# Optimization experiments

Measured on AMD Instinct MI355X. Metric: run time of the kernel, lower is better.

## Reference

```python
import jax, jax.numpy as jnp
import numpy as np
from jax import lax

H_ENC = 64
H_DEC = 128
PRED_STEPS = 30


def _run_lstm_last(x, Wih, Whh, bih, bhh):
    """Batched LSTM (batch_first), returns last hidden state. x: [N, T, I] -> [N, H]."""
    N = x.shape[0]
    H = Whh.shape[1]
    xg = jnp.einsum('nti,gi->ntg', x, Wih) + bih  # [N, T, 4H], input projection hoisted

    def step(carry, g_t):
        h, c = carry
        gates = g_t + h @ Whh.T + bhh
        i, f, g, o = jnp.split(gates, 4, axis=-1)  # torch gate order i,f,g,o
        c = jax.nn.sigmoid(f) * c + jax.nn.sigmoid(i) * jnp.tanh(g)
        h = jax.nn.sigmoid(o) * jnp.tanh(c)
        return (h, c), None

    z = jnp.zeros((N, H), x.dtype)
    (h, _), _ = lax.scan(step, (z, z), jnp.swapaxes(xg, 0, 1))
    return h


def setup_inputs() -> dict:
    key = jax.random.key(0)
    ks = jax.random.split(key, 20)
    B, T, NMAX = 2048, 50, 16
    s = 0.1
    inp = {
        'train_agent': jax.random.normal(ks[0], (B, T, 2), jnp.float32),
        'neighbour': jax.random.normal(ks[1], (B, NMAX, T, 2), jnp.float32),
        'neighbour_counts': jax.random.randint(ks[2], (B,), 0, NMAX + 1),
        # agent encoder LSTM(2 -> 64)
        'Wih_a': jax.random.normal(ks[3], (4 * H_ENC, 2), jnp.float32) * s,
        'Whh_a': jax.random.normal(ks[4], (4 * H_ENC, H_ENC), jnp.float32) * s,
        'bih_a': jax.random.normal(ks[5], (4 * H_ENC,), jnp.float32) * s,
        'bhh_a': jax.random.normal(ks[6], (4 * H_ENC,), jnp.float32) * s,
        # neighbour encoder LSTM(2 -> 64)
        'Wih_n': jax.random.normal(ks[7], (4 * H_ENC, 2), jnp.float32) * s,
        'Whh_n': jax.random.normal(ks[8], (4 * H_ENC, H_ENC), jnp.float32) * s,
        'bih_n': jax.random.normal(ks[9], (4 * H_ENC,), jnp.float32) * s,
        'bhh_n': jax.random.normal(ks[10], (4 * H_ENC,), jnp.float32) * s,
        # decoder LSTMCell(128 -> 128)
        'Wih_d': jax.random.normal(ks[11], (4 * H_DEC, H_DEC), jnp.float32) * s,
        'Whh_d': jax.random.normal(ks[12], (4 * H_DEC, H_DEC), jnp.float32) * s,
        'bih_d': jax.random.normal(ks[13], (4 * H_DEC,), jnp.float32) * s,
        'bhh_d': jax.random.normal(ks[14], (4 * H_DEC,), jnp.float32) * s,
        # embedding_pos Linear(128 -> 2)
        'Wpos': jax.random.normal(ks[15], (2, H_DEC), jnp.float32) * s,
        'bpos': jax.random.normal(ks[16], (2,), jnp.float32) * s,
    }
    return inp


def reference(train_agent, neighbour, neighbour_counts,
              Wih_a, Whh_a, bih_a, bhh_a,
              Wih_n, Whh_n, bih_n, bhh_n,
              Wih_d, Whh_d, bih_d, bhh_d,
              Wpos, bpos):
    B, NMAX, T, _ = neighbour.shape

    # agent encoder: last hidden state  [B, 64]
    agent_emb = _run_lstm_last(train_agent, Wih_a, Whh_a, bih_a, bhh_a)

    # neighbour encoder over all padded neighbour sequences  [B*NMAX, 64]
    n_enc = _run_lstm_last(neighbour.reshape(B * NMAX, T, 2),
                           Wih_n, Whh_n, bih_n, bhh_n).reshape(B, NMAX, H_ENC)
    valid = jnp.arange(NMAX)[None, :] < neighbour_counts[:, None]  # [B, NMAX]
    neg_inf = jnp.asarray(-jnp.inf, n_enc.dtype)
    n_max = jnp.max(jnp.where(valid[:, :, None], n_enc, neg_inf), axis=1)  # [B, 64]
    neigh_emb = jnp.where((neighbour_counts > 0)[:, None], n_max,
                          jnp.zeros((), n_enc.dtype))

    # decoder: LSTMCell fed its own hidden state as input, 30 steps
    h0 = jnp.concatenate([agent_emb, neigh_emb], axis=1)  # [B, 128]
    c0 = jnp.zeros_like(h0)

    def dec_step(carry, _):
        h, c = carry
        gates = h @ Wih_d.T + bih_d + h @ Whh_d.T + bhh_d  # input == hidden == h
        i, f, g, o = jnp.split(gates, 4, axis=-1)
        c_new = jax.nn.sigmoid(f) * c + jax.nn.sigmoid(i) * jnp.tanh(g)
        h_new = jax.nn.sigmoid(o) * jnp.tanh(c_new)
        pred = h_new @ Wpos.T + bpos  # [B, 2]
        return (h_new, c_new), pred

    _, preds = lax.scan(dec_step, (h0, c0), None, length=PRED_STEPS)  # [30, B, 2]
    return jnp.swapaxes(preds, 0, 1)  # [B, 30, 2]
```

## Files before the change

kernel.cpp:

```cpp
#include <hip/hip_runtime.h>
#include <stdint.h>


#define T_SEQ 50
#define PRED_STEPS 30
#define NMAX 16

typedef float v2f __attribute__((ext_vector_type(2)));
typedef float v4f __attribute__((ext_vector_type(4)));
typedef short v8s __attribute__((ext_vector_type(8)));

#define L2E 1.44269504f
#define L2E2 2.88539008f

static constexpr size_t OFF_AEMB  = 0;
static constexpr size_t OFF_NENC  = 131072;
static constexpr size_t OFF_IDX   = 2228224;
static constexpr size_t OFF_PACKA = 2490368;
static constexpr size_t OFF_PACKN = 2498560;
static constexpr size_t OFF_WDP   = 2506752;
static constexpr size_t OFF_WDB   = 2539520;

__device__ __forceinline__ float frcp(float x) { return __builtin_amdgcn_rcpf(x); }
#if __has_builtin(__builtin_amdgcn_exp2f)
__device__ __forceinline__ float fexp2(float x) { return __builtin_amdgcn_exp2f(x); }
#else
__device__ __forceinline__ float fexp2(float x) { return exp2f(x); }
#endif
__device__ __forceinline__ unsigned bf16rne(float f) {
  unsigned u = __float_as_uint(f);
  u += 0x7fff + ((u >> 16) & 1);
  return u >> 16;
}
__device__ __forceinline__ v4f mfma16(v8s a, v8s b, v4f c) {
  return __builtin_amdgcn_mfma_f32_16x16x32_bf16(a, b, c, 0, 0, 0);
}

__device__ __forceinline__ float cell_update(float iv, float fv, float gv,
                                             float ov, float& cref) {
  float ef = fexp2(-fv);
  float ei = fexp2(-iv);
  float eg = fexp2(-gv);
  float t1 = (1.f + ei) * (1.f + eg);
  float rD = frcp((1.f + ef) * t1);
  float sf = t1 * rD;
  float u  = (1.f - eg) * ((1.f + ef) * rD);
  float cn = fmaf(sf, cref, u);
  cref = cn;
  float eo = fexp2(-ov);
  float ec = fexp2(fminf(-L2E2 * cn, 60.f));
  return (1.f - ec) * frcp((1.f + eo) * (1.f + ec));
}

__device__ __forceinline__ uint4 pack8(const float* __restrict__ p, float gs) {
  float4 w0 = *(const float4*)p;
  float4 w1 = *(const float4*)(p + 4);
  uint4 o;
  o.x = bf16rne(w0.x * gs) | (bf16rne(w0.y * gs) << 16);
  o.y = bf16rne(w0.z * gs) | (bf16rne(w0.w * gs) << 16);
  o.z = bf16rne(w1.x * gs) | (bf16rne(w1.y * gs) << 16);
  o.w = bf16rne(w1.z * gs) | (bf16rne(w1.w * gs) << 16);
  return o;
}
__device__ __forceinline__ uint4 pack8sum(const float* __restrict__ pa,
                                          const float* __restrict__ pb, float gs) {
  float4 a0 = *(const float4*)pa, a1 = *(const float4*)(pa + 4);
  float4 b0 = *(const float4*)pb, b1 = *(const float4*)(pb + 4);
  uint4 o;
  o.x = bf16rne((a0.x + b0.x) * gs) | (bf16rne((a0.y + b0.y) * gs) << 16);
  o.y = bf16rne((a0.z + b0.z) * gs) | (bf16rne((a0.w + b0.w) * gs) << 16);
  o.z = bf16rne((a1.x + b1.x) * gs) | (bf16rne((a1.y + b1.y) * gs) << 16);
  o.w = bf16rne((a1.z + b1.z) * gs) | (bf16rne((a1.w + b1.w) * gs) << 16);
  return o;
}

__global__ void prep_kernel(const float* __restrict__ Whh_a, const float* __restrict__ Whh_n,
                            const float* __restrict__ Wih_d, const float* __restrict__ Whh_d,
                            const float* __restrict__ bih_d, const float* __restrict__ bhh_d,
                            uint4* __restrict__ packA, uint4* __restrict__ packN,
                            uint4* __restrict__ packD, float* __restrict__ bd,
                            int* __restrict__ idxb) {
  const int b = blockIdx.x;
  {
    const int gi = b * 256 + threadIdx.x;
    for (int i = gi; i < 32768; i += 12288) idxb[i] = -1;
    if (gi == 0) idxb[32768] = 0;
  }
  if (b < 16) {
    const int which = b >> 3;
    const float* Whh = which ? Whh_n : Whh_a;
    uint4* dst = which ? packN : packA;
    const int idx = (b & 7) * 256 + threadIdx.x;
    const int lane = idx & 63, c = idx >> 6;
    const int kh = c & 1, g = (c >> 1) & 3, w = c >> 3;
    const float gs = (g == 2) ? L2E2 : L2E;
    const int row = g * 64 + 16 * w + (lane & 15);
    const int kb = kh * 32 + (lane >> 4) * 8;
    dst[c * 64 + lane] = pack8(Whh + row * 64 + kb, gs);
  } else {
    const int idx = (b - 16) * 256 + threadIdx.x;
    const int lane = idx & 63, c = idx >> 6;
    const int kh = c & 3, i = (c >> 2) & 1, wv = c >> 3;
    const int g = wv & 3, q = wv >> 2;
    const float gs = (g == 2) ? L2E2 : L2E;
    const int ju = q * 32 + i * 16 + (lane & 15);
    const int row = g * 128 + ju;
    const int kb = kh * 32 + (lane >> 4) * 8;
    packD[c * 64 + lane] = pack8sum(Wih_d + row * 128 + kb, Whh_d + row * 128 + kb, gs);
    if (b < 18) {
      int iB = (b - 16) * 256 + threadIdx.x;
      float s = ((iB >> 7) == 2) ? L2E2 : L2E;
      bd[iB] = (bih_d[iB] + bhh_d[iB]) * s;
    }
  }
}

__global__ void compact_kernel(const int* __restrict__ cnts, int* __restrict__ idxb) {
  const int b = blockIdx.x * 256 + threadIdx.x;
  if (b >= 2048) return;
  int cnt = cnts[b];
  cnt = cnt < 0 ? 0 : (cnt > NMAX ? NMAX : cnt);
  if (cnt == 0) return;
  int pos = atomicAdd(idxb + 32768, cnt);
  for (int j = 0; j < cnt; ++j) idxb[pos + j] = b * NMAX + j;
}

__global__ __launch_bounds__(256, 4) void enc_mfma_kernel(
    const float* __restrict__ xA, const float* __restrict__ xN,
    const v8s* __restrict__ packA, const v8s* __restrict__ packN,
    const float* __restrict__ Wih_a, const float* __restrict__ bih_a, const float* __restrict__ bhh_a,
    const float* __restrict__ Wih_n, const float* __restrict__ bih_n, const float* __restrict__ bhh_n,
    const int* __restrict__ idxb,
    float* __restrict__ outA, float* __restrict__ outN) {
  __shared__ unsigned short hph[2304];
  __shared__ float xst[1600];
  __shared__ int sidx[16];
  const int tid = threadIdx.x, lane = tid & 63, wv = tid >> 6;
  const int nb = blockIdx.x;
  const bool isA = nb >= 2048;
  const int s0 = (isA ? nb - 2048 : nb) * 16;

  if (!isA && s0 >= idxb[32768]) return;

  const float* xsrc = isA ? xA : xN;
  const v8s* pk = isA ? packA : packN;
  const float* Wih = isA ? Wih_a : Wih_n;
  const float* bih = isA ? bih_a : bih_n;
  const float* bhh = isA ? bhh_a : bhh_n;
  float* outp = isA ? outA : outN;

  v8s B[4][2];
#pragma unroll
  for (int g = 0; g < 4; ++g)
#pragma unroll
    for (int kh = 0; kh < 2; ++kh)
      B[g][kh] = pk[(wv * 8 + g * 2 + kh) * 64 + lane];

  const int jc = lane & 15, qc = lane >> 4;
  float wi0[4], wi1[4], bs[4];
#pragma unroll
  for (int g = 0; g < 4; ++g) {
    const float gs = (g == 2) ? L2E2 : L2E;
    int n = g * 64 + 16 * wv + jc;
    wi0[g] = Wih[n * 2 + 0] * gs;
    wi1[g] = Wih[n * 2 + 1] * gs;
    bs[g] = (bih[n] + bhh[n]) * gs;
  }

  {
    if (tid < 16) sidx[tid] = isA ? (s0 + tid) : idxb[s0 + tid];
    for (int i = tid; i < 576; i += 256) ((unsigned*)hph)[i] = 0;
    __syncthreads();
    for (int i = tid; i < 400; i += 256) {
      int slot = i / 25, j = i - slot * 25;
      int sq = sidx[slot];
      const float4* xb = (const float4*)(xsrc + (size_t)(sq < 0 ? 0 : sq) * 100);
      ((float4*)xst)[i] = xb[j];
    }
  }
  __syncthreads();

  const int ms = lane & 15, ks = lane >> 4;
  float cst[4] = {0.f, 0.f, 0.f, 0.f};
  float h[4];

  auto enc_step = [&](int t, int rb, int wb) {
    v4f a4[4];
#pragma unroll
    for (int r = 0; r < 4; ++r) {
      v2f xv = *(const __shared__ v2f*)&xst[(qc * 4 + r) * 100 + 2 * t];
#pragma unroll
      for (int g = 0; g < 4; ++g)
        a4[g][r] = fmaf(wi1[g], xv.y, fmaf(wi0[g], xv.x, bs[g]));
    }

#pragma unroll
    for (int kh = 0; kh < 2; ++kh) {
      v8s Ahi = *(const __shared__ v8s*)&hph[rb + ms * 72 + kh * 32 + ks * 8];
#pragma unroll
      for (int g = 0; g < 4; ++g)
        a4[g] = mfma16(Ahi, B[g][kh], a4[g]);
    }

#pragma unroll
    for (int r = 0; r < 4; ++r) {
      h[r] = cell_update(a4[0][r], a4[1][r], a4[2][r], a4[3][r], cst[r]);
      hph[wb + (qc * 4 + r) * 72 + 16 * wv + jc] =
          (unsigned short)bf16rne(h[r]);
    }
    __syncthreads();
  };

  for (int t2 = 0; t2 < T_SEQ; t2 += 2) {
    enc_step(t2 + 0, 0, 1152);
    enc_step(t2 + 1, 1152, 0);
  }

#pragma unroll
  for (int r = 0; r < 4; ++r) {
    int sq = sidx[qc * 4 + r];
    if (sq >= 0)
      outp[(size_t)sq * 64 + 16 * wv + jc] = h[r];
  }
}

__global__ __launch_bounds__(1024, 4) void dec_mfma_kernel(
    const v8s* __restrict__ pkd, const float* __restrict__ bd,
    const float* __restrict__ aemb, const float* __restrict__ nenc,
    const int* __restrict__ cnts, const float* __restrict__ Wpos,
    const float* __restrict__ bpos, float* __restrict__ out) {
  __shared__ unsigned short hph[2176];
  __shared__ float gbuf[4][8][132];
  __shared__ float ppart[16][2];
  __shared__ float pbuf[480];
  const int tid = threadIdx.x, lane = tid & 63, wv = tid >> 6;
  const int jc = lane & 15, qc = lane >> 4;
  const int g = wv & 3, q = wv >> 2;
  const int s0 = blockIdx.x * 8;

  v8s B[2][4];
  float bs[2];
#pragma unroll
  for (int i = 0; i < 2; ++i) {
#pragma unroll
    for (int kh = 0; kh < 4; ++kh)
      B[i][kh] = pkd[(wv * 8 + i * 4 + kh) * 64 + lane];
    bs[i] = bd[g * 128 + q * 32 + i * 16 + jc];
  }

  const int cu = (wv & 1) * 64 + lane;
  const int sq = wv >> 1;
  const float wp0 = Wpos[cu], wp1 = Wpos[128 + cu];
  const float bp0 = bpos[0], bp1 = bpos[1];

  for (int i = tid; i < 2048; i += 1024) {
    int row = i >> 7, unit = i & 127;
    unsigned hiw = 0;
    if (row < 8) {
      float v;
      if (unit < 64) {
        v = aemb[(size_t)(s0 + row) * 64 + unit];
      } else {
        int cnt = cnts[s0 + row];
        float m = -1e30f;
#pragma unroll
        for (int n = 0; n < NMAX; ++n) {
          float val = nenc[((size_t)((s0 + row) * NMAX + n)) * 64 + (unit - 64)];
          m = (n < cnt) ? fmaxf(m, val) : m;
        }
        v = (cnt > 0) ? m : 0.f;
      }
      hiw = bf16rne(v);
    }
    hph[row * 136 + unit] = (unsigned short)hiw;
  }
  float cst = 0.f;
  __syncthreads();

  for (int t = 0; t < PRED_STEPS; ++t) {
    v4f acc[2];
#pragma unroll
    for (int i = 0; i < 2; ++i)
      acc[i] = (v4f){bs[i], bs[i], bs[i], bs[i]};
#pragma unroll
    for (int kh = 0; kh < 4; ++kh) {
      v8s Ahi = *(const __shared__ v8s*)&hph[jc * 136 + kh * 32 + qc * 8];
#pragma unroll
      for (int i = 0; i < 2; ++i)
        acc[i] = mfma16(Ahi, B[i][kh], acc[i]);
    }

    if (qc < 2) {
#pragma unroll
      for (int i = 0; i < 2; ++i)
#pragma unroll
        for (int r = 0; r < 4; ++r)
          gbuf[g][qc * 4 + r][q * 32 + i * 16 + jc] = acc[i][r];
    }
    __syncthreads();

    float gI = gbuf[0][sq][cu];
    float gF = gbuf[1][sq][cu];
    float gG = gbuf[2][sq][cu];
    float gO = gbuf[3][sq][cu];
    float h = cell_update(gI, gF, gG, gO, cst);

    hph[sq * 136 + cu] = (unsigned short)bf16rne(h);

    float p0 = h * wp0;
    float p1 = h * wp1;
#pragma unroll
    for (int off = 32; off > 0; off >>= 1) {
      p0 += __shfl_xor(p0, off, 64);
      p1 += __shfl_xor(p1, off, 64);
    }
    if (lane == 0) { ppart[wv][0] = p0; ppart[wv][1] = p1; }
    __syncthreads();

    if (tid < 16) {
      int s = tid >> 1, cc = tid & 1;
      pbuf[s * 60 + t * 2 + cc] =
          ppart[2 * s][cc] + ppart[2 * s + 1][cc] + (cc ? bp1 : bp0);
    }
  }
  __syncthreads();
  if (tid < 480) out[(size_t)s0 * 60 + tid] = pbuf[tid];
}

extern "C" void kernel_launch(void* const* d_in, const int* in_sizes, int n_in,
                              void* d_out, int out_size, void* d_ws, size_t ws_size,
                              hipStream_t stream) {
  (void)in_sizes; (void)n_in; (void)out_size; (void)ws_size;
  const float* xA    = (const float*)d_in[0];
  const float* xN    = (const float*)d_in[1];
  const int*   cnts  = (const int*)d_in[2];
  const float* Wih_a = (const float*)d_in[3];
  const float* Whh_a = (const float*)d_in[4];
  const float* bih_a = (const float*)d_in[5];
  const float* bhh_a = (const float*)d_in[6];
  const float* Wih_n = (const float*)d_in[7];
  const float* Whh_n = (const float*)d_in[8];
  const float* bih_n = (const float*)d_in[9];
  const float* bhh_n = (const float*)d_in[10];
  const float* Wih_d = (const float*)d_in[11];
  const float* Whh_d = (const float*)d_in[12];
  const float* bih_d = (const float*)d_in[13];
  const float* bhh_d = (const float*)d_in[14];
  const float* Wpos  = (const float*)d_in[15];
  const float* bpos  = (const float*)d_in[16];
  float* out = (float*)d_out;
  float* wsf = (float*)d_ws;
  int* idxb = (int*)(wsf + OFF_IDX);

  prep_kernel<<<48, 256, 0, stream>>>(Whh_a, Whh_n, Wih_d, Whh_d, bih_d, bhh_d,
                                      (uint4*)(wsf + OFF_PACKA),
                                      (uint4*)(wsf + OFF_PACKN),
                                      (uint4*)(wsf + OFF_WDP), wsf + OFF_WDB,
                                      idxb);
  compact_kernel<<<8, 256, 0, stream>>>(cnts, idxb);
  enc_mfma_kernel<<<2176, 256, 0, stream>>>(
      xA, xN,
      (const v8s*)(wsf + OFF_PACKA), (const v8s*)(wsf + OFF_PACKN),
      Wih_a, bih_a, bhh_a, Wih_n, bih_n, bhh_n, idxb,
      wsf + OFF_AEMB, wsf + OFF_NENC);
  dec_mfma_kernel<<<256, 1024, 0, stream>>>(
      (const v8s*)(wsf + OFF_WDP), wsf + OFF_WDB,
      wsf + OFF_AEMB, wsf + OFF_NENC, cnts,
      Wpos, bpos, out);
}
```

Measured before the change: 220.2 us.

## Restructure decoder so each wave owns all four gates of its units

The decoder drops from 16 to 8 waves per block, and each wave now computes all four gate tiles (i,f,g,o) for 16 hidden units. The cell update then runs directly from MFMA accumulators, without staging gates through shared memory. The hidden state is double-buffered in LDS and the prediction partials are kept per step and reduced once at the end, so each step needs one barrier instead of two. In exchange each thread holds more weight fragments in registers and does more serial MFMAs, while the decoder is a small part of the whole pipeline.

```diff
diff --git a/kernel.cpp b/kernel.cpp
--- a/kernel.cpp
+++ b/kernel.cpp
@@ -224,107 +224,110 @@
   }
 }
 
-__global__ __launch_bounds__(1024, 4) void dec_mfma_kernel(
+__global__ __launch_bounds__(512, 2) void dec_mfma_kernel(
     const v8s* __restrict__ pkd, const float* __restrict__ bd,
     const float* __restrict__ aemb, const float* __restrict__ nenc,
     const int* __restrict__ cnts, const float* __restrict__ Wpos,
     const float* __restrict__ bpos, float* __restrict__ out) {
-  __shared__ unsigned short hph[2176];
-  __shared__ float gbuf[4][8][132];
-  __shared__ float ppart[16][2];
-  __shared__ float pbuf[480];
+  __shared__ unsigned short hph[2][2176];
+  __shared__ float pall[3840];
   const int tid = threadIdx.x, lane = tid & 63, wv = tid >> 6;
   const int jc = lane & 15, qc = lane >> 4;
-  const int g = wv & 3, q = wv >> 2;
   const int s0 = blockIdx.x * 8;
 
-  v8s B[2][4];
-  float bs[2];
-#pragma unroll
-  for (int i = 0; i < 2; ++i) {
+  v8s B[4][4];
+  float bs[4];
+#pragma unroll
+  for (int g = 0; g < 4; ++g) {
 #pragma unroll
     for (int kh = 0; kh < 4; ++kh)
-      B[i][kh] = pkd[(wv * 8 + i * 4 + kh) * 64 + lane];
-    bs[i] = bd[g * 128 + q * 32 + i * 16 + jc];
-  }
-
-  const int cu = (wv & 1) * 64 + lane;
-  const int sq = wv >> 1;
-  const float wp0 = Wpos[cu], wp1 = Wpos[128 + cu];
+      B[g][kh] = pkd[(((wv >> 1) * 4 + g) * 8 + (wv & 1) * 4 + kh) * 64 + lane];
+    bs[g] = bd[g * 128 + wv * 16 + jc];
+  }
+  const float wp0 = Wpos[wv * 16 + jc];
+  const float wp1 = Wpos[128 + wv * 16 + jc];
   const float bp0 = bpos[0], bp1 = bpos[1];
 
-  for (int i = tid; i < 2048; i += 1024) {
+  for (int i = tid; i < 2176; i += 512) ((unsigned*)hph)[i] = 0;
+  __syncthreads();
+
+  for (int i = tid; i < 1024; i += 512) {
     int row = i >> 7, unit = i & 127;
-    unsigned hiw = 0;
-    if (row < 8) {
-      float v;
-      if (unit < 64) {
-        v = aemb[(size_t)(s0 + row) * 64 + unit];
-      } else {
-        int cnt = cnts[s0 + row];
-        float m = -1e30f;
-#pragma unroll
-        for (int n = 0; n < NMAX; ++n) {
-          float val = nenc[((size_t)((s0 + row) * NMAX + n)) * 64 + (unit - 64)];
-          m = (n < cnt) ? fmaxf(m, val) : m;
-        }
-        v = (cnt > 0) ? m : 0.f;
+    float v;
+    if (unit < 64) {
+      v = aemb[(size_t)(s0 + row) * 64 + unit];
+    } else {
+      int cnt = cnts[s0 + row];
+      float m = -1e30f;
+#pragma unroll
+    for (int n = 0; n < NMAX; ++n) {
+        float val = nenc[((size_t)((s0 + row) * NMAX + n)) * 64 + (unit - 64)];
+        m = (n < cnt) ? fmaxf(m, val) : m;
       }
-      hiw = bf16rne(v);
-    }
-    hph[row * 136 + unit] = (unsigned short)hiw;
-  }
-  float cst = 0.f;
+      v = (cnt > 0) ? m : 0.f;
+    }
+    hph[0][row * 136 + unit] = (unsigned short)bf16rne(v);
+  }
+  float cst[4] = {0.f, 0.f, 0.f, 0.f};
   __syncthreads();
 
   for (int t = 0; t < PRED_STEPS; ++t) {
-    v4f acc[2];
-#pragma unroll
-    for (int i = 0; i < 2; ++i)
-      acc[i] = (v4f){bs[i], bs[i], bs[i], bs[i]};
+    const int rb = t & 1, wb = rb ^ 1;
+    v4f acc[4];
+#pragma unroll
+    for (int g = 0; g < 4; ++g)
+      acc[g] = (v4f){bs[g], bs[g], bs[g], bs[g]};
 #pragma unroll
     for (int kh = 0; kh < 4; ++kh) {
-      v8s Ahi = *(const __shared__ v8s*)&hph[jc * 136 + kh * 32 + qc * 8];
-#pragma unroll
-      for (int i = 0; i < 2; ++i)
-        acc[i] = mfma16(Ahi, B[i][kh], acc[i]);
-    }
+      v8s Ahi = *(const __shared__ v8s*)&hph[rb][jc * 136 + kh * 32 + qc * 8];
+#pragma unroll
+      for (int g = 0; g < 4; ++g)
+        acc[g] = mfma16(Ahi, B[g][kh], acc[g]);
+    }
+
+    float hr[4];
+#pragma unroll
+    for (int r = 0; r < 4; ++r)
+      hr[r] = cell_update(acc[0][r], acc[1][r], acc[2][r], acc[3][r], cst[r]);
 
     if (qc < 2) {
 #pragma unroll
-      for (int i = 0; i < 2; ++i)
-#pragma unroll
-        for (int r = 0; r < 4; ++r)
-          gbuf[g][qc * 4 + r][q * 32 + i * 16 + jc] = acc[i][r];
+      for (int r = 0; r < 4; ++r)
+        hph[wb][(qc * 4 + r) * 136 + wv * 16 + jc] =
+            (unsigned short)bf16rne(hr[r]);
+    }
+
+    float pr0[4], pr1[4];
+#pragma unroll
+    for (int r = 0; r < 4; ++r) { pr0[r] = hr[r] * wp0; pr1[r] = hr[r] * wp1; }
+#pragma unroll
+    for (int off = 1; off < 16; off <<= 1) {
+#pragma unroll
+      for (int r = 0; r < 4; ++r) {
+        pr0[r] += __shfl_xor(pr0[r], off, 64);
+        pr1[r] += __shfl_xor(pr1[r], off, 64);
+      }
+    }
+    if (jc == 0 && qc < 2) {
+#pragma unroll
+      for (int r = 0; r < 4; ++r) {
+        int s = qc * 4 + r;
+        pall[t * 128 + wv * 16 + s * 2 + 0] = pr0[r];
+        pall[t * 128 + wv * 16 + s * 2 + 1] = pr1[r];
+      }
     }
     __syncthreads();
-
-    float gI = gbuf[0][sq][cu];
-    float gF = gbuf[1][sq][cu];
-    float gG = gbuf[2][sq][cu];
-    float gO = gbuf[3][sq][cu];
-    float h = cell_update(gI, gF, gG, gO, cst);
-
-    hph[sq * 136 + cu] = (unsigned short)bf16rne(h);
-
-    float p0 = h * wp0;
-    float p1 = h * wp1;
-#pragma unroll
-    for (int off = 32; off > 0; off >>= 1) {
-      p0 += __shfl_xor(p0, off, 64);
-      p1 += __shfl_xor(p1, off, 64);
-    }
-    if (lane == 0) { ppart[wv][0] = p0; ppart[wv][1] = p1; }
-    __syncthreads();
-
-    if (tid < 16) {
-      int s = tid >> 1, cc = tid & 1;
-      pbuf[s * 60 + t * 2 + cc] =
-          ppart[2 * s][cc] + ppart[2 * s + 1][cc] + (cc ? bp1 : bp0);
-    }
-  }
-  __syncthreads();
-  if (tid < 480) out[(size_t)s0 * 60 + tid] = pbuf[tid];
+  }
+
+  if (tid < 480) {
+    int s = tid / 60, r60 = tid - s * 60;
+    int t = r60 >> 1, c = r60 & 1;
+    float a = c ? bp1 : bp0;
+#pragma unroll
+    for (int w = 0; w < 8; ++w)
+      a += pall[t * 128 + w * 16 + s * 2 + c];
+    out[(size_t)(s0 + s) * 60 + r60] = a;
+  }
 }
 
 extern "C" void kernel_launch(void* const* d_in, const int* in_sizes, int n_in,
@@ -363,7 +366,7 @@
       (const v8s*)(wsf + OFF_PACKA), (const v8s*)(wsf + OFF_PACKN),
       Wih_a, bih_a, bhh_a, Wih_n, bih_n, bhh_n, idxb,
       wsf + OFF_AEMB, wsf + OFF_NENC);
-  dec_mfma_kernel<<<256, 1024, 0, stream>>>(
+  dec_mfma_kernel<<<256, 512, 0, stream>>>(
       (const v8s*)(wsf + OFF_WDP), wsf + OFF_WDB,
       wsf + OFF_AEMB, wsf + OFF_NENC, cnts,
       Wpos, bpos, out);
```

Result: slower. 226.9 us (+3.1%).
